# Kernel tuning notes

Hardware: AMD Instinct MI355X
Metric: run time of the kernel (lower is better)

## Reference

```python
import jax, jax.numpy as jnp
import numpy as np

NMS_THRESH = 0.5
SCORE_THRESH = 0.05
MAX_DET = 300


def _iou_one_vs_all(box, boxes):
    # box: [4] (x1,y1,x2,y2); boxes: [N,4]
    x1 = jnp.maximum(box[0], boxes[:, 0])
    y1 = jnp.maximum(box[1], boxes[:, 1])
    x2 = jnp.minimum(box[2], boxes[:, 2])
    y2 = jnp.minimum(box[3], boxes[:, 3])
    inter = jnp.maximum(x2 - x1, 0.0) * jnp.maximum(y2 - y1, 0.0)
    area_a = (box[2] - box[0]) * (box[3] - box[1])
    area_b = (boxes[:, 2] - boxes[:, 0]) * (boxes[:, 3] - boxes[:, 1])
    union = area_a + area_b - inter
    return inter / jnp.maximum(union, 1e-8)


def _nms_single_class(boxes, scores):
    # Greedy NMS with max_output_size=MAX_DET, matching tf.image.non_max_suppression
    # after score-threshold prefiltering. boxes:[N,4], scores:[N].
    s0 = jnp.where(scores > SCORE_THRESH, scores, -jnp.inf)

    def step(s, _):
        i = jnp.argmax(s)
        si = s[i]
        sel = jnp.isfinite(si)  # False once no candidates remain
        iou = _iou_one_vs_all(boxes[i], boxes)
        s = jnp.where(sel & (iou > NMS_THRESH), -jnp.inf, s)
        s = s.at[i].set(-jnp.inf)
        return s, (i, si, sel)

    _, (idx, sv, sel) = jax.lax.scan(step, s0, None, length=MAX_DET)
    # unselected slots carry -inf score
    return idx.astype(jnp.int32), jnp.where(sel, sv, -jnp.inf)


def _filter_one_image(boxes, classification, other):
    # boxes:[N,4], classification:[N,C], other:[N,D]
    C = classification.shape[1]
    # class-specific NMS (class_specific_filter=True, nms=True)
    idx, sv = jax.vmap(lambda c: _nms_single_class(boxes, classification[:, c]))(
        jnp.arange(C))  # each [C, MAX_DET]
    labels = jnp.broadcast_to(jnp.arange(C)[:, None], idx.shape)
    cand_scores = sv.reshape(-1)          # [C*MAX_DET]
    cand_idx = idx.reshape(-1)
    cand_lab = labels.reshape(-1)
    # global top-k over all per-class survivors
    top_s, top_i = jax.lax.top_k(cand_scores, MAX_DET)
    sel_idx = cand_idx[top_i]
    sel_lab = cand_lab[top_i]
    valid = jnp.isfinite(top_s)
    # pad invalid slots with -1 (matches tf.pad(..., constant_values=-1))
    out_boxes = jnp.where(valid[:, None], boxes[sel_idx], -1.0)
    out_scores = jnp.where(valid, top_s, -1.0)
    out_labels = jnp.where(valid, sel_lab, -1).astype(jnp.int32)
    out_other = jnp.where(valid[:, None], other[sel_idx], -1.0)
    return out_boxes, out_scores, out_labels, out_other


def setup_inputs() -> dict:
    key = jax.random.key(0)
    k1, k2, k3, k4 = jax.random.split(key, 4)
    B, N, C, D = 16, 50000, 8, 2
    xy = jax.random.uniform(k1, (B, N, 2), jnp.float32, 0.0, 512.0)
    wh = jax.random.uniform(k2, (B, N, 2), jnp.float32, 4.0, 100.0)
    boxes = jnp.concatenate([xy, xy + wh], axis=-1)  # valid (x1,y1,x2,y2)
    classification = jax.random.uniform(k3, (B, N, C), jnp.float32)
    other = jax.random.normal(k4, (B, N, D), jnp.float32)
    return {"boxes": boxes, "classification": classification, "other": other}


def reference(boxes, classification, other):
    # tf.map_fn over batch -> vmap over batch
    return jax.vmap(_filter_one_image)(boxes, classification, other)
```

## Files before the change

kernel.cpp:

```cpp
#include <hip/hip_runtime.h>
#include <math.h>
#include <stdint.h>

#define NB 16
#define NN 50000
#define NC 8
#define ND 2
#define MAX_DET 300
#define NMS_T 0.5f
#define SCORE_T 0.05f
#define CAP 1024
#define CUTBIN 252
#define LBUF 128
#define CHUNK 128
#define NT 512
#define NPI (NN * NC)
#define CBLK 32
#define F4PB (NPI / 4 / CBLK)

typedef unsigned long long u64;

__device__ __forceinline__ float neg_inf() { return -__builtin_inff(); }

__device__ __forceinline__ bool iou_gt(float ax1, float ay1, float ax2, float ay2,
                                       float area_a,
                                       float bx1, float by1, float bx2, float by2) {
    float x1 = fmaxf(ax1, bx1), y1 = fmaxf(ay1, by1);
    float x2 = fminf(ax2, bx2), y2 = fminf(ay2, by2);
    float inter = __fmul_rn(fmaxf(__fsub_rn(x2, x1), 0.0f),
                            fmaxf(__fsub_rn(y2, y1), 0.0f));
    float area_b = __fmul_rn(__fsub_rn(bx2, bx1), __fsub_rn(by2, by1));
    float uni = __fsub_rn(__fadd_rn(area_a, area_b), inter);
    return inter > __fmul_rn(0.5f, fmaxf(uni, 1e-8f));
}

__device__ __forceinline__ u64 score_key(float s, int n) {
    unsigned u = __float_as_uint(s);
    u ^= (u & 0x80000000u) ? 0xFFFFFFFFu : 0x80000000u;
    return ((u64)u << 32) | (unsigned)(~(unsigned)n);
}

__device__ __forceinline__ u64 shfl_xor_u64(u64 v, int m) {
    unsigned lo = (unsigned)v, hi = (unsigned)(v >> 32);
    lo = __shfl_xor(lo, m, 64);
    hi = __shfl_xor(hi, m, 64);
    return ((u64)hi << 32) | lo;
}

__global__ __launch_bounds__(1024) void compact_kernel(
    const float* __restrict__ cls, int* __restrict__ cnt_g,
    u64* __restrict__ cand)
{
    const int b = blockIdx.x >> 5, t32 = blockIdx.x & 31;
    const int tid = threadIdx.x;
    __shared__ u64 buf[8][LBUF];
    __shared__ int lcnt[8], gbase[8];
    if (tid < 8) lcnt[tid] = 0;
    __syncthreads();

    const float4* c4 = (const float4*)(cls + (size_t)b * NPI);
    const int f0 = t32 * F4PB, fend = f0 + F4PB;

    for (int f = f0 + tid; f < fend; f += 1024) {
        float4 v = c4[f];
        int cb = (f & 1) * 4;
        int n = f >> 1;
        float vv[4] = {v.x, v.y, v.z, v.w};
        #pragma unroll
        for (int k = 0; k < 4; ++k) {
            float s = vv[k];
            if (s > SCORE_T) {
                int bn = (int)(s * 256.0f); if (bn > 255) bn = 255;
                if (bn >= CUTBIN) {
                    int c = cb + k;
                    int pos = atomicAdd(&lcnt[c], 1);
                    u64 key = score_key(s, n);
                    if (pos < LBUF) buf[c][pos] = key;
                    else {
                        int gp = atomicAdd(&cnt_g[b * 8 + c], 1);
                        if (gp < CAP) cand[(size_t)(b * 8 + c) * CAP + gp] = key;
                    }
                }
            }
        }
    }
    __syncthreads();
    if (tid < 8) {
        int m = lcnt[tid]; if (m > LBUF) m = LBUF;
        gbase[tid] = atomicAdd(&cnt_g[b * 8 + tid], m);
    }
    __syncthreads();
    for (int c = 0; c < 8; ++c) {
        int m = lcnt[c]; if (m > LBUF) m = LBUF;
        int gb = gbase[c];
        for (int i = tid; i < m; i += 1024) {
            int gp = gb + i;
            if (gp < CAP) cand[(size_t)(b * 8 + c) * CAP + gp] = buf[c][i];
        }
    }
}

__global__ __launch_bounds__(NT) void nms_fused(
    const float* __restrict__ boxes, const float* __restrict__ cls,
    const u64* __restrict__ cand, const int* __restrict__ cnt_g,
    int* __restrict__ sel_idx, float* __restrict__ sel_score)
{
    const int bc = blockIdx.x;
    const int b = bc >> 3, c = bc & 7;
    const int tid = threadIdx.x;
    const int lane = tid & 63, widx = tid >> 6;
    const float4* bx4 = (const float4*)(boxes + (size_t)b * NN * 4);
    const float* sr = cls + (size_t)b * NN * NC + c;
    const u64* g = cand + (size_t)bc * CAP;
    int* si = sel_idx + bc * MAX_DET;
    float* ss = sel_score + bc * MAX_DET;

    __shared__ u64 keys[CAP];
    __shared__ float4 cbox2[2][CHUNK];
    __shared__ float  carea2[2][CHUNK];
    __shared__ int    cidx2[2][CHUNK];
    __shared__ float  cscore2[2][CHUNK];
    __shared__ unsigned M32[4][CHUNK];
    __shared__ unsigned presup4[4][CHUNK];
    __shared__ u64 accmask_s[2];
    __shared__ float4 abox[MAX_DET];
    __shared__ float aarea[MAX_DET];
    __shared__ unsigned bm[(NN + 31) / 32];
    __shared__ float rv[NT];
    __shared__ int   ri[NT];
    __shared__ float sboxsh[5];

    const int cnt = cnt_g[bc];
    const bool full_fb = (cnt > CAP);
    const int inSet = cnt < CAP ? cnt : CAP;

    int n_acc = 0;
    if (!full_fb) {
        const int p0 = widx * 128 + lane, p1 = p0 + 64;
        u64 v0 = (p0 < cnt) ? g[p0] : 0ull;
        u64 v1 = (p1 < cnt) ? g[p1] : 0ull;

        #pragma unroll
        for (int k = 2; k <= 128; k <<= 1) {
            #pragma unroll
            for (int j = k >> 1; j > 0; j >>= 1) {
                if (j == 64) {
                    bool dir = ((p0 & k) == 0);
                    if ((v0 < v1) == dir) { u64 t = v0; v0 = v1; v1 = t; }
                } else {
                    bool lower = ((lane & j) == 0);
                    bool dir0 = ((p0 & k) == 0);
                    bool dir1 = ((p1 & k) == 0);
                    u64 o0 = shfl_xor_u64(v0, j);
                    u64 mx0 = v0 > o0 ? v0 : o0, mn0 = v0 > o0 ? o0 : v0;
                    v0 = (lower == dir0) ? mx0 : mn0;
                    u64 o1 = shfl_xor_u64(v1, j);
                    u64 mx1 = v1 > o1 ? v1 : o1, mn1 = v1 > o1 ? o1 : v1;
                    v1 = (lower == dir1) ? mx1 : mn1;
                }
            }
        }
        for (int k = 256; k <= CAP; k <<= 1) {
            keys[p0] = v0; keys[p1] = v1;
            __syncthreads();
            for (int j = k >> 1; j >= 128; j >>= 1) {
                int p = tid;
                int i = 2 * p - (p & (j - 1));
                int ix = i + j;
                bool dir = ((i & k) == 0);
                u64 a = keys[i], b2 = keys[ix];
                if ((a < b2) == dir) { keys[i] = b2; keys[ix] = a; }
                __syncthreads();
            }
            v0 = keys[p0]; v1 = keys[p1];
            {
                bool dir = ((p0 & k) == 0);
                if ((v0 < v1) == dir) { u64 t = v0; v0 = v1; v1 = t; }
            }
            #pragma unroll
            for (int j = 32; j > 0; j >>= 1) {
                bool lower = ((lane & j) == 0);
                bool dir = ((p0 & k) == 0);
                u64 o0 = shfl_xor_u64(v0, j);
                u64 mx0 = v0 > o0 ? v0 : o0, mn0 = v0 > o0 ? o0 : v0;
                v0 = (lower == dir) ? mx0 : mn0;
                u64 o1 = shfl_xor_u64(v1, j);
                u64 mx1 = v1 > o1 ? v1 : o1, mn1 = v1 > o1 ? o1 : v1;
                v1 = (lower == dir) ? mx1 : mn1;
            }
            __syncthreads();
        }
        keys[p0] = v0; keys[p1] = v1;
        __syncthreads();

        if (tid < CHUNK && tid < inSet) {
            u64 key = keys[tid];
            int idx = (int)(~(unsigned)key);
            unsigned u = (unsigned)(key >> 32);
            unsigned uo = (u & 0x80000000u) ? (u ^ 0x80000000u) : (~u);
            float4 bb = bx4[idx];
            cbox2[0][tid] = bb;
            carea2[0][tid] = __fmul_rn(__fsub_rn(bb.z, bb.x), __fsub_rn(bb.w, bb.y));
            cidx2[0][tid] = idx; cscore2[0][tid] = __uint_as_float(uo);
        }
        __syncthreads();

        int base = 0, cur = 0;
        while (n_acc < MAX_DET && base < inSet) {
            int m = inSet - base; if (m > CHUNK) m = CHUNK;

            {
                int i = tid & (CHUNK - 1);
                int q = tid >> 7;
                if (i < m) {
                    float4 B = cbox2[cur][i];
                    unsigned p = 0;
                    int t = q;
                    for (; t + 12 < n_acc; t += 16) {
                        float4 A0 = abox[t];      float r0 = aarea[t];
                        float4 A1 = abox[t + 4];  float r1 = aarea[t + 4];
                        float4 A2 = abox[t + 8];  float r2 = aarea[t + 8];
                        float4 A3 = abox[t + 12]; float r3 = aarea[t + 12];
                        bool s0 = iou_gt(A0.x,A0.y,A0.z,A0.w,r0,B.x,B.y,B.z,B.w);
                        bool s1 = iou_gt(A1.x,A1.y,A1.z,A1.w,r1,B.x,B.y,B.z,B.w);
                        bool s2 = iou_gt(A2.x,A2.y,A2.z,A2.w,r2,B.x,B.y,B.z,B.w);
                        bool s3 = iou_gt(A3.x,A3.y,A3.z,A3.w,r3,B.x,B.y,B.z,B.w);
                        if (s0 || s1 || s2 || s3) { p = 1; break; }
                    }
                    if (!p) {
                        for (; t < n_acc; t += 4) {
                            float4 A = abox[t];
                            if (iou_gt(A.x,A.y,A.z,A.w,aarea[t],
                                       B.x,B.y,B.z,B.w)) { p = 1; break; }
                        }
                    }
                    presup4[q][i] = p;
                    unsigned bits = 0;
                    int j0 = q * 32;
                    int jend = i - j0; if (jend > 32) jend = 32;
                    for (int jj = 0; jj < jend; ++jj) {
                        int j = j0 + jj;
                        float4 A = cbox2[cur][j];
                        if (iou_gt(A.x,A.y,A.z,A.w,carea2[cur][j],
                                   B.x,B.y,B.z,B.w))
                            bits |= 1u << jj;
                    }
                    M32[q][i] = bits;
                }
            }
            __syncthreads();

            int nbase = base + m;
            if (tid < 64) {
                u64 a0 = 0, a1 = 0;
                int ngroups = (m + 63) >> 6;
                for (int gg = 0; gg < ngroups; ++gg) {
                    int i = gg * 64 + tid;
                    unsigned pe = 1; u64 mg = 0;
                    if (i < m) {
                        pe = presup4[0][i] | presup4[1][i] | presup4[2][i] | presup4[3][i];
                        mg = (u64)M32[2 * gg][i] | ((u64)M32[2 * gg + 1][i] << 32);
                        if (gg > 0) {
                            u64 w0 = (u64)M32[0][i] | ((u64)M32[1][i] << 32);
                            if (w0 & a0) pe = 1;
                        }
                    }
                    u64 rem = ~__ballot(pe != 0);
                    u64 accw = 0;
                    while (rem) {
                        int l = __builtin_ctzll(rem);
                        accw |= 1ull << l;
                        rem &= ~(1ull << l);
                        u64 supm = __ballot(((mg >> l) & 1ull) != 0);
                        rem &= ~supm;
                    }
                    if (gg == 0) a0 = accw; else a1 = accw;
                }
                if (tid == 0) { accmask_s[0] = a0; accmask_s[1] = a1; }
            } else if (nbase < inSet) {
                int w = tid - 64;
                if (w < CHUNK && nbase + w < inSet) {
                    u64 key = keys[nbase + w];
                    int idx = (int)(~(unsigned)key);
                    unsigned u = (unsigned)(key >> 32);
                    unsigned uo = (u & 0x80000000u) ? (u ^ 0x80000000u) : (~u);
                    float4 bb = bx4[idx];
                    cbox2[cur ^ 1][w] = bb;
                    carea2[cur ^ 1][w] = __fmul_rn(__fsub_rn(bb.z, bb.x), __fsub_rn(bb.w, bb.y));
                    cidx2[cur ^ 1][w] = idx; cscore2[cur ^ 1][w] = __uint_as_float(uo);
                }
            }
            __syncthreads();

            u64 a0 = accmask_s[0], a1 = accmask_s[1];
            int add = __popcll(a0) + __popcll(a1);
            if (tid < m) {
                int gg = tid >> 6, o = tid & 63;
                u64 aw = (gg == 0) ? a0 : a1;
                if ((aw >> o) & 1ull) {
                    int rank = (gg > 0) ? __popcll(a0) : 0;
                    rank += __popcll(aw & ((1ull << o) - 1ull));
                    int pos = n_acc + rank;
                    if (pos < MAX_DET) {
                        abox[pos] = cbox2[cur][tid]; aarea[pos] = carea2[cur][tid];
                        si[pos] = cidx2[cur][tid]; ss[pos] = cscore2[cur][tid];
                    }
                }
            }
            n_acc += add; if (n_acc > MAX_DET) n_acc = MAX_DET;
            base = nbase; cur ^= 1;
            __syncthreads();
        }
    }

    const bool part_fb = (!full_fb) && (n_acc < MAX_DET);

    if (full_fb || part_fb) {
        const int BMW = (NN + 31) / 32;
        for (int i = tid; i < BMW; i += NT) bm[i] = 0u;
        __syncthreads();
        if (full_fb) {
            n_acc = 0;
        } else {
            for (int n = tid; n < NN; n += NT) {
                float4 bbn = bx4[n];
                int s = 0;
                for (int t = 0; t < n_acc; ++t) {
                    float4 A = abox[t];
                    if (iou_gt(A.x, A.y, A.z, A.w, aarea[t],
                               bbn.x, bbn.y, bbn.z, bbn.w)) s = 1;
                }
                if (s) atomicOr(&bm[n >> 5], 1u << (n & 31));
            }
        }
        __syncthreads();

        for (int k = n_acc; k < MAX_DET; ++k) {
            float bv = neg_inf(); int bi = 0x7fffffff;
            for (int n = tid; n < NN; n += NT) {
                if (!((bm[n >> 5] >> (n & 31)) & 1u)) {
                    float v = sr[(size_t)n * NC];
                    if (v > SCORE_T && v > bv) { bv = v; bi = n; }
                }
            }
            rv[tid] = bv; ri[tid] = bi;
            __syncthreads();
            for (int s = NT / 2; s > 0; s >>= 1) {
                if (tid < s) {
                    float ov = rv[tid + s]; int oi = ri[tid + s];
                    if (ov > rv[tid] || (ov == rv[tid] && oi < ri[tid])) { rv[tid] = ov; ri[tid] = oi; }
                }
                __syncthreads();
            }
            float mval = rv[0]; int midx = ri[0];
            if (mval == neg_inf()) {
                for (int kk = k + tid; kk < MAX_DET; kk += NT) { si[kk] = 0; ss[kk] = neg_inf(); }
                break;
            }
            if (tid == 0) {
                si[k] = midx; ss[k] = mval;
                float4 sb = bx4[midx];
                sboxsh[0] = sb.x; sboxsh[1] = sb.y; sboxsh[2] = sb.z; sboxsh[3] = sb.w;
                sboxsh[4] = __fmul_rn(__fsub_rn(sb.z, sb.x), __fsub_rn(sb.w, sb.y));
            }
            __syncthreads();
            float ax1 = sboxsh[0], ay1 = sboxsh[1], ax2 = sboxsh[2], ay2 = sboxsh[3];
            float area_a = sboxsh[4];
            for (int n = tid; n < NN; n += NT) {
                float4 bbn = bx4[n];
                if (iou_gt(ax1, ay1, ax2, ay2, area_a,
                           bbn.x, bbn.y, bbn.z, bbn.w))
                    atomicOr(&bm[n >> 5], 1u << (n & 31));
            }
            __syncthreads();
        }
    } else {
        for (int kk = n_acc + tid; kk < MAX_DET; kk += NT) { si[kk] = 0; ss[kk] = neg_inf(); }
    }
}

__global__ __launch_bounds__(1024) void topk_kernel(
    const float* __restrict__ boxes, const float* __restrict__ other,
    const int* __restrict__ sel_idx, const float* __restrict__ sel_score,
    float* __restrict__ out)
{
    const int b = blockIdx.x;
    const int tid = threadIdx.x;
    __shared__ u64 keys[4096];

    for (int i = tid; i < 4096; i += 1024) {
        int c = i >> 9, o = i & 511;
        u64 key = 0ull;
        if (o < MAX_DET) {
            int m = c * MAX_DET + o;
            float v = sel_score[b * NC * MAX_DET + m];
            unsigned u = __float_as_uint(v);
            u ^= (u & 0x80000000u) ? 0xFFFFFFFFu : 0x80000000u;
            key = ((u64)u << 32) | (unsigned)(~(unsigned)m);
        }
        keys[i] = key;
    }

    for (int seg = 1024; seg <= 4096; seg <<= 1) {
        int half = seg >> 1;
        __syncthreads();
        {
            int p = tid;
            int s = p / (half >> 1), t = p % (half >> 1);
            int i0 = s * seg + half + t;
            int i1 = s * seg + seg - 1 - t;
            u64 a = keys[i0]; keys[i0] = keys[i1]; keys[i1] = a;
        }
        __syncthreads();
        for (int j = half; j > 0; j >>= 1) {
            for (int p = tid; p < 2048; p += 1024) {
                int i = 2 * p - (p & (j - 1));
                int ix = i + j;
                u64 a = keys[i], bq = keys[ix];
                if (a < bq) { keys[i] = bq; keys[ix] = a; }
            }
            if (j >= 128) __syncthreads(); else __threadfence_block();
        }
    }
    __syncthreads();

    const float4* bx4 = (const float4*)(boxes + (size_t)b * NN * 4);
    const float*  ot  = other + (size_t)b * NN * ND;
    float* ob = out;
    float* os = out + NB * MAX_DET * 4;
    float* ol = os + NB * MAX_DET;
    float* oo = ol + NB * MAX_DET;

    for (int k = tid; k < MAX_DET; k += 1024) {
        u64 key = keys[k];
        unsigned u = (unsigned)(key >> 32);
        unsigned uo = (u & 0x80000000u) ? (u ^ 0x80000000u) : (u ^ 0xFFFFFFFFu);
        float score = __uint_as_float(uo);
        bool valid = isfinite(score);
        float b0=-1.f,b1=-1.f,b2=-1.f,b3=-1.f,scv=-1.f,lab=-1.f,o0=-1.f,o1=-1.f;
        if (valid) {
            int m = (int)(~(unsigned)key);
            int c = m / MAX_DET, slot = m - c * MAX_DET;
            int n = sel_idx[(b * NC + c) * MAX_DET + slot];
            float4 bb = bx4[n];
            b0 = bb.x; b1 = bb.y; b2 = bb.z; b3 = bb.w;
            scv = score; lab = (float)c;
            o0 = ot[n * ND + 0]; o1 = ot[n * ND + 1];
        }
        int base = b * MAX_DET + k;
        ob[base * 4 + 0] = b0; ob[base * 4 + 1] = b1;
        ob[base * 4 + 2] = b2; ob[base * 4 + 3] = b3;
        os[base] = scv; ol[base] = lab;
        oo[base * 2 + 0] = o0; oo[base * 2 + 1] = o1;
    }
}

extern "C" void kernel_launch(void* const* d_in, const int* in_sizes, int n_in,
                              void* d_out, int out_size, void* d_ws, size_t ws_size,
                              hipStream_t stream) {
    const float* boxes = (const float*)d_in[0];
    const float* cls   = (const float*)d_in[1];
    const float* other = (const float*)d_in[2];
    float* out = (float*)d_out;

    int* cnt_g = (int*)d_ws;
    u64* cand  = (u64*)(cnt_g + NB * NC * 2);
    int* sel_idx = (int*)(cand + (size_t)NB * NC * CAP);
    float* sel_score = (float*)(sel_idx + NB * NC * MAX_DET);

    hipMemsetAsync(cnt_g, 0, NB * NC * sizeof(int), stream);
    compact_kernel<<<NB * CBLK, 1024, 0, stream>>>(cls, cnt_g, cand);
    nms_fused<<<NB * NC, NT, 0, stream>>>(boxes, cls, cand, cnt_g,
                                          sel_idx, sel_score);
    topk_kernel<<<NB, 1024, 0, stream>>>(boxes, other, sel_idx, sel_score, out);
}
```

Measured before the change: 72.74 us.

## Resolve first 512 NMS candidates in one block-wide suppression-matrix pass

```diff
diff --git a/kernel.cpp b/kernel.cpp
--- a/kernel.cpp
+++ b/kernel.cpp
@@ -12,6 +12,7 @@
 #define CAP 1024
 #define CUTBIN 252
 #define LBUF 128
+#define BIGM 512
 #define CHUNK 128
 #define NT 512
 #define NPI (NN * NC)
@@ -116,19 +117,28 @@
     float* ss = sel_score + bc * MAX_DET;
 
     __shared__ u64 keys[CAP];
-    __shared__ float4 cbox2[2][CHUNK];
-    __shared__ float  carea2[2][CHUNK];
-    __shared__ int    cidx2[2][CHUNK];
-    __shared__ float  cscore2[2][CHUNK];
-    __shared__ unsigned M32[4][CHUNK];
-    __shared__ unsigned presup4[4][CHUNK];
+    __shared__ __align__(16) char regA[32768];
+    __shared__ __align__(16) char regB[14336];
+    __shared__ u64 accs_s[8];
     __shared__ u64 accmask_s[2];
     __shared__ float4 abox[MAX_DET];
     __shared__ float aarea[MAX_DET];
-    __shared__ unsigned bm[(NN + 31) / 32];
-    __shared__ float rv[NT];
-    __shared__ int   ri[NT];
     __shared__ float sboxsh[5];
+
+    u64 (*Mword)[BIGM] = (u64(*)[BIGM])regA;
+    unsigned* bm = (unsigned*)regA;
+    float* rv = (float*)(regA + 6256);
+    int*   ri = (int*)(regA + 8304);
+    float4* cbig   = (float4*)regB;
+    float* careabig = (float*)(regB + 8192);
+    int*   cidxbig  = (int*)(regB + 10240);
+    float* csbig    = (float*)(regB + 12288);
+    float4 (*cbox2)[CHUNK] = (float4(*)[CHUNK])regB;
+    float*  carea2 = (float*)(regB + 4096);
+    int*    cidx2  = (int*)(regB + 5120);
+    float*  cscore2= (float*)(regB + 6144);
+    unsigned (*M32)[CHUNK] = (unsigned(*)[CHUNK])(regB + 7168);
+    unsigned (*presup4)[CHUNK] = (unsigned(*)[CHUNK])(regB + 9216);
 
     const int cnt = cnt_g[bc];
     const bool full_fb = (cnt > CAP);
@@ -139,7 +149,6 @@
         const int p0 = widx * 128 + lane, p1 = p0 + 64;
         u64 v0 = (p0 < cnt) ? g[p0] : 0ull;
         u64 v1 = (p1 < cnt) ? g[p1] : 0ull;
-
         #pragma unroll
         for (int k = 2; k <= 128; k <<= 1) {
             #pragma unroll
@@ -193,123 +202,192 @@
         keys[p0] = v0; keys[p1] = v1;
         __syncthreads();
 
-        if (tid < CHUNK && tid < inSet) {
+        const int stage = inSet < BIGM ? inSet : BIGM;
+        if (tid < stage) {
             u64 key = keys[tid];
             int idx = (int)(~(unsigned)key);
             unsigned u = (unsigned)(key >> 32);
             unsigned uo = (u & 0x80000000u) ? (u ^ 0x80000000u) : (~u);
             float4 bb = bx4[idx];
-            cbox2[0][tid] = bb;
-            carea2[0][tid] = __fmul_rn(__fsub_rn(bb.z, bb.x), __fsub_rn(bb.w, bb.y));
-            cidx2[0][tid] = idx; cscore2[0][tid] = __uint_as_float(uo);
-        }
-        __syncthreads();
-
-        int base = 0, cur = 0;
-        while (n_acc < MAX_DET && base < inSet) {
-            int m = inSet - base; if (m > CHUNK) m = CHUNK;
-
-            {
-                int i = tid & (CHUNK - 1);
-                int q = tid >> 7;
-                if (i < m) {
-                    float4 B = cbox2[cur][i];
-                    unsigned p = 0;
-                    int t = q;
-                    for (; t + 12 < n_acc; t += 16) {
-                        float4 A0 = abox[t];      float r0 = aarea[t];
-                        float4 A1 = abox[t + 4];  float r1 = aarea[t + 4];
-                        float4 A2 = abox[t + 8];  float r2 = aarea[t + 8];
-                        float4 A3 = abox[t + 12]; float r3 = aarea[t + 12];
-                        bool s0 = iou_gt(A0.x,A0.y,A0.z,A0.w,r0,B.x,B.y,B.z,B.w);
-                        bool s1 = iou_gt(A1.x,A1.y,A1.z,A1.w,r1,B.x,B.y,B.z,B.w);
-                        bool s2 = iou_gt(A2.x,A2.y,A2.z,A2.w,r2,B.x,B.y,B.z,B.w);
-                        bool s3 = iou_gt(A3.x,A3.y,A3.z,A3.w,r3,B.x,B.y,B.z,B.w);
-                        if (s0 || s1 || s2 || s3) { p = 1; break; }
+            cbig[tid] = bb;
+            careabig[tid] = __fmul_rn(__fsub_rn(bb.z, bb.x), __fsub_rn(bb.w, bb.y));
+            cidxbig[tid] = idx; csbig[tid] = __uint_as_float(uo);
+        }
+        __syncthreads();
+
+        {
+            const int r = tid;
+            const int jmax = (widx + 1) << 6;
+            float4 B = cbig[r < stage ? r : 0];
+            float  Ba = careabig[r < stage ? r : 0];
+            (void)Ba;
+            u64 bits = 0;
+            for (int j = 0; j < jmax; ++j) {
+                if (j < r && r < stage) {
+                    float4 A = cbig[j];
+                    if (iou_gt(A.x, A.y, A.z, A.w, careabig[j],
+                               B.x, B.y, B.z, B.w))
+                        bits |= 1ull << (j & 63);
+                }
+                if ((j & 63) == 63) { Mword[j >> 6][r] = bits; bits = 0; }
+            }
+        }
+        __syncthreads();
+
+        if (tid < 64) {
+            u64 acc[8];
+            #pragma unroll
+            for (int gg = 0; gg < 8; ++gg) acc[gg] = 0ull;
+            const int stage = inSet < BIGM ? inSet : BIGM;
+            for (int gg = 0; gg < 8; ++gg) {
+                int i = gg * 64 + lane;
+                unsigned pe = (i < stage) ? 0u : 1u;
+                u64 mg = 0;
+                if (i < stage) {
+                    mg = Mword[gg][i];
+                    for (int h = 0; h < gg; ++h)
+                        if (Mword[h][i] & acc[h]) pe = 1;
+                }
+                u64 rem = ~__ballot(pe != 0);
+                u64 accw = 0;
+                while (rem) {
+                    int l = __builtin_ctzll(rem);
+                    accw |= 1ull << l;
+                    rem &= ~(1ull << l);
+                    u64 supm = __ballot(((mg >> l) & 1ull) != 0);
+                    rem &= ~supm;
+                }
+                acc[gg] = accw;
+            }
+            if (lane == 0) {
+                #pragma unroll
+                for (int gg = 0; gg < 8; ++gg) accs_s[gg] = acc[gg];
+            }
+        }
+        __syncthreads();
+
+        {
+            int total_acc = 0;
+            #pragma unroll
+            for (int gg = 0; gg < 8; ++gg) total_acc += __popcll(accs_s[gg]);
+            int gg = widx, o = 0;
+            gg = tid >> 6; o = tid & 63;
+            u64 aw = accs_s[gg];
+            if ((aw >> o) & 1ull) {
+                int rank = 0;
+                for (int h = 0; h < gg; ++h) rank += __popcll(accs_s[h]);
+                rank += __popcll(aw & ((1ull << o) - 1ull));
+                if (rank < MAX_DET) {
+                    abox[rank] = cbig[tid]; aarea[rank] = careabig[tid];
+                    si[rank] = cidxbig[tid]; ss[rank] = csbig[tid];
+                }
+            }
+            n_acc = total_acc < MAX_DET ? total_acc : MAX_DET;
+        }
+        __syncthreads();
+
+        int base = BIGM, cur = 0;
+        if (n_acc < MAX_DET && base < inSet) {
+            if (tid < CHUNK && base + tid < inSet) {
+                u64 key = keys[base + tid];
+                int idx = (int)(~(unsigned)key);
+                unsigned u = (unsigned)(key >> 32);
+                unsigned uo = (u & 0x80000000u) ? (u ^ 0x80000000u) : (~u);
+                float4 bb = bx4[idx];
+                cbox2[0][tid] = bb;
+                carea2[0 * CHUNK + tid] = __fmul_rn(__fsub_rn(bb.z, bb.x), __fsub_rn(bb.w, bb.y));
+                cidx2[0 * CHUNK + tid] = idx; cscore2[0 * CHUNK + tid] = __uint_as_float(uo);
+            }
+            __syncthreads();
+            while (n_acc < MAX_DET && base < inSet) {
+                int m = inSet - base; if (m > CHUNK) m = CHUNK;
+                {
+                    int i = tid & (CHUNK - 1);
+                    int q = tid >> 7;
+                    if (i < m) {
+                        float4 B = cbox2[cur][i];
+                        unsigned p = 0;
+                        for (int t = q; t < n_acc; t += 4) {
+                            float4 A = abox[t];
+                            if (iou_gt(A.x, A.y, A.z, A.w, aarea[t],
+                                       B.x, B.y, B.z, B.w)) { p = 1; break; }
+                        }
+                        presup4[q][i] = p;
+                        unsigned bits = 0;
+                        int j0 = q * 32;
+                        int jend = i - j0; if (jend > 32) jend = 32;
+                        for (int jj = 0; jj < jend; ++jj) {
+                            int j = j0 + jj;
+                            float4 A = cbox2[cur][j];
+                            if (iou_gt(A.x, A.y, A.z, A.w, carea2[cur * CHUNK + j],
+                                       B.x, B.y, B.z, B.w))
+                                bits |= 1u << jj;
+                        }
+                        M32[q][i] = bits;
                     }
-                    if (!p) {
-                        for (; t < n_acc; t += 4) {
-                            float4 A = abox[t];
-                            if (iou_gt(A.x,A.y,A.z,A.w,aarea[t],
-                                       B.x,B.y,B.z,B.w)) { p = 1; break; }
+                }
+                __syncthreads();
+                int nbase = base + m;
+                if (tid < 64) {
+                    u64 a0 = 0, a1 = 0;
+                    int ngroups = (m + 63) >> 6;
+                    for (int gg = 0; gg < ngroups; ++gg) {
+                        int i = gg * 64 + lane;
+                        unsigned pe = 1; u64 mg = 0;
+                        if (i < m) {
+                            pe = presup4[0][i] | presup4[1][i] | presup4[2][i] | presup4[3][i];
+                            mg = (u64)M32[2 * gg][i] | ((u64)M32[2 * gg + 1][i] << 32);
+                            if (gg > 0) {
+                                u64 w0 = (u64)M32[0][i] | ((u64)M32[1][i] << 32);
+                                if (w0 & a0) pe = 1;
+                            }
+                        }
+                        u64 rem = ~__ballot(pe != 0);
+                        u64 accw = 0;
+                        while (rem) {
+                            int l = __builtin_ctzll(rem);
+                            accw |= 1ull << l;
+                            rem &= ~(1ull << l);
+                            u64 supm = __ballot(((mg >> l) & 1ull) != 0);
+                            rem &= ~supm;
+                        }
+                        if (gg == 0) a0 = accw; else a1 = accw;
+                    }
+                    if (lane == 0) { accmask_s[0] = a0; accmask_s[1] = a1; }
+                } else if (nbase < inSet) {
+                    int w = tid - 64;
+                    if (w < CHUNK && nbase + w < inSet) {
+                        u64 key = keys[nbase + w];
+                        int idx = (int)(~(unsigned)key);
+                        unsigned u = (unsigned)(key >> 32);
+                        unsigned uo = (u & 0x80000000u) ? (u ^ 0x80000000u) : (~u);
+                        float4 bb = bx4[idx];
+                        cbox2[cur ^ 1][w] = bb;
+                        carea2[(cur ^ 1) * CHUNK + w] = __fmul_rn(__fsub_rn(bb.z, bb.x), __fsub_rn(bb.w, bb.y));
+                        cidx2[(cur ^ 1) * CHUNK + w] = idx;
+                        cscore2[(cur ^ 1) * CHUNK + w] = __uint_as_float(uo);
+                    }
+                }
+                __syncthreads();
+                u64 a0 = accmask_s[0], a1 = accmask_s[1];
+                int add = __popcll(a0) + __popcll(a1);
+                if (tid < m) {
+                    int gg = tid >> 6, o = tid & 63;
+                    u64 aw = (gg == 0) ? a0 : a1;
+                    if ((aw >> o) & 1ull) {
+                        int rank = (gg > 0) ? __popcll(a0) : 0;
+                        rank += __popcll(aw & ((1ull << o) - 1ull));
+                        int pos = n_acc + rank;
+                        if (pos < MAX_DET) {
+                            abox[pos] = cbox2[cur][tid]; aarea[pos] = carea2[cur * CHUNK + tid];
+                            si[pos] = cidx2[cur * CHUNK + tid]; ss[pos] = cscore2[cur * CHUNK + tid];
                         }
                     }
-                    presup4[q][i] = p;
-                    unsigned bits = 0;
-                    int j0 = q * 32;
-                    int jend = i - j0; if (jend > 32) jend = 32;
-                    for (int jj = 0; jj < jend; ++jj) {
-                        int j = j0 + jj;
-                        float4 A = cbox2[cur][j];
-                        if (iou_gt(A.x,A.y,A.z,A.w,carea2[cur][j],
-                                   B.x,B.y,B.z,B.w))
-                            bits |= 1u << jj;
-                    }
-                    M32[q][i] = bits;
-                }
-            }
-            __syncthreads();
-
-            int nbase = base + m;
-            if (tid < 64) {
-                u64 a0 = 0, a1 = 0;
-                int ngroups = (m + 63) >> 6;
-                for (int gg = 0; gg < ngroups; ++gg) {
-                    int i = gg * 64 + tid;
-                    unsigned pe = 1; u64 mg = 0;
-                    if (i < m) {
-                        pe = presup4[0][i] | presup4[1][i] | presup4[2][i] | presup4[3][i];
-                        mg = (u64)M32[2 * gg][i] | ((u64)M32[2 * gg + 1][i] << 32);
-                        if (gg > 0) {
-                            u64 w0 = (u64)M32[0][i] | ((u64)M32[1][i] << 32);
-                            if (w0 & a0) pe = 1;
-                        }
-                    }
-                    u64 rem = ~__ballot(pe != 0);
-                    u64 accw = 0;
-                    while (rem) {
-                        int l = __builtin_ctzll(rem);
-                        accw |= 1ull << l;
-                        rem &= ~(1ull << l);
-                        u64 supm = __ballot(((mg >> l) & 1ull) != 0);
-                        rem &= ~supm;
-                    }
-                    if (gg == 0) a0 = accw; else a1 = accw;
-                }
-                if (tid == 0) { accmask_s[0] = a0; accmask_s[1] = a1; }
-            } else if (nbase < inSet) {
-                int w = tid - 64;
-                if (w < CHUNK && nbase + w < inSet) {
-                    u64 key = keys[nbase + w];
-                    int idx = (int)(~(unsigned)key);
-                    unsigned u = (unsigned)(key >> 32);
-                    unsigned uo = (u & 0x80000000u) ? (u ^ 0x80000000u) : (~u);
-                    float4 bb = bx4[idx];
-                    cbox2[cur ^ 1][w] = bb;
-                    carea2[cur ^ 1][w] = __fmul_rn(__fsub_rn(bb.z, bb.x), __fsub_rn(bb.w, bb.y));
-                    cidx2[cur ^ 1][w] = idx; cscore2[cur ^ 1][w] = __uint_as_float(uo);
-                }
-            }
-            __syncthreads();
-
-            u64 a0 = accmask_s[0], a1 = accmask_s[1];
-            int add = __popcll(a0) + __popcll(a1);
-            if (tid < m) {
-                int gg = tid >> 6, o = tid & 63;
-                u64 aw = (gg == 0) ? a0 : a1;
-                if ((aw >> o) & 1ull) {
-                    int rank = (gg > 0) ? __popcll(a0) : 0;
-                    rank += __popcll(aw & ((1ull << o) - 1ull));
-                    int pos = n_acc + rank;
-                    if (pos < MAX_DET) {
-                        abox[pos] = cbox2[cur][tid]; aarea[pos] = carea2[cur][tid];
-                        si[pos] = cidx2[cur][tid]; ss[pos] = cscore2[cur][tid];
-                    }
-                }
-            }
-            n_acc += add; if (n_acc > MAX_DET) n_acc = MAX_DET;
-            base = nbase; cur ^= 1;
-            __syncthreads();
+                }
+                n_acc += add; if (n_acc > MAX_DET) n_acc = MAX_DET;
+                base = nbase; cur ^= 1;
+                __syncthreads();
+            }
         }
     }
 
```

New measurement: 128.4 us. 76.6% more time.

## Replace global-atomic candidate compaction with per-tile slots and in-NMS prefix scan

Applied to the files above, without the earlier changes.

```diff
diff --git a/kernel.cpp b/kernel.cpp
--- a/kernel.cpp
+++ b/kernel.cpp
@@ -12,11 +12,11 @@
 #define CAP 1024
 #define CUTBIN 252
 #define LBUF 128
+#define NTILE32 32
 #define CHUNK 128
 #define NT 512
 #define NPI (NN * NC)
-#define CBLK 32
-#define F4PB (NPI / 4 / CBLK)
+#define F4PB (NPI / 4 / NTILE32)
 
 typedef unsigned long long u64;
 
@@ -48,13 +48,13 @@
 }
 
 __global__ __launch_bounds__(1024) void compact_kernel(
-    const float* __restrict__ cls, int* __restrict__ cnt_g,
+    const float* __restrict__ cls, int* __restrict__ tcnt_g,
     u64* __restrict__ cand)
 {
     const int b = blockIdx.x >> 5, t32 = blockIdx.x & 31;
     const int tid = threadIdx.x;
     __shared__ u64 buf[8][LBUF];
-    __shared__ int lcnt[8], gbase[8];
+    __shared__ int lcnt[8];
     if (tid < 8) lcnt[tid] = 0;
     __syncthreads();
 
@@ -74,35 +74,24 @@
                 if (bn >= CUTBIN) {
                     int c = cb + k;
                     int pos = atomicAdd(&lcnt[c], 1);
-                    u64 key = score_key(s, n);
-                    if (pos < LBUF) buf[c][pos] = key;
-                    else {
-                        int gp = atomicAdd(&cnt_g[b * 8 + c], 1);
-                        if (gp < CAP) cand[(size_t)(b * 8 + c) * CAP + gp] = key;
-                    }
+                    if (pos < LBUF) buf[c][pos] = score_key(s, n);
                 }
             }
         }
     }
     __syncthreads();
-    if (tid < 8) {
-        int m = lcnt[tid]; if (m > LBUF) m = LBUF;
-        gbase[tid] = atomicAdd(&cnt_g[b * 8 + tid], m);
-    }
-    __syncthreads();
-    for (int c = 0; c < 8; ++c) {
-        int m = lcnt[c]; if (m > LBUF) m = LBUF;
-        int gb = gbase[c];
-        for (int i = tid; i < m; i += 1024) {
-            int gp = gb + i;
-            if (gp < CAP) cand[(size_t)(b * 8 + c) * CAP + gp] = buf[c][i];
-        }
+    {
+        int c = tid >> 7, i = tid & (LBUF - 1);
+        int m = lcnt[c];
+        if (i < (m < LBUF ? m : LBUF))
+            cand[(size_t)(((b * 8 + c) * NTILE32) + t32) * LBUF + i] = buf[c][i];
+        if (i == 0) tcnt_g[(b * 8 + c) * NTILE32 + t32] = m;
     }
 }
 
 __global__ __launch_bounds__(NT) void nms_fused(
     const float* __restrict__ boxes, const float* __restrict__ cls,
-    const u64* __restrict__ cand, const int* __restrict__ cnt_g,
+    const u64* __restrict__ cand, const int* __restrict__ tcnt_g,
     int* __restrict__ sel_idx, float* __restrict__ sel_score)
 {
     const int bc = blockIdx.x;
@@ -111,11 +100,12 @@
     const int lane = tid & 63, widx = tid >> 6;
     const float4* bx4 = (const float4*)(boxes + (size_t)b * NN * 4);
     const float* sr = cls + (size_t)b * NN * NC + c;
-    const u64* g = cand + (size_t)bc * CAP;
     int* si = sel_idx + bc * MAX_DET;
     float* ss = sel_score + bc * MAX_DET;
 
     __shared__ u64 keys[CAP];
+    __shared__ int tcnt_s[NTILE32], toff_s[NTILE32];
+    __shared__ int sh_total, sh_ovf;
     __shared__ float4 cbox2[2][CHUNK];
     __shared__ float  carea2[2][CHUNK];
     __shared__ int    cidx2[2][CHUNK];
@@ -130,16 +120,37 @@
     __shared__ int   ri[NT];
     __shared__ float sboxsh[5];
 
-    const int cnt = cnt_g[bc];
-    const bool full_fb = (cnt > CAP);
+    if (tid < 64) {
+        int v = (lane < NTILE32) ? tcnt_g[bc * NTILE32 + lane] : 0;
+        int incl = v;
+        #pragma unroll
+        for (int d = 1; d < 32; d <<= 1) {
+            int o = __shfl_up(incl, d, 64);
+            if (lane >= d) incl += o;
+        }
+        if (lane < NTILE32) { tcnt_s[lane] = v; toff_s[lane] = incl - v; }
+        u64 ov = __ballot(lane < NTILE32 && v > LBUF);
+        if (lane == 31) { sh_total = incl; sh_ovf = (ov != 0); }
+    }
+    __syncthreads();
+    const int cnt = sh_total;
+    const bool full_fb = sh_ovf || (cnt > CAP);
     const int inSet = cnt < CAP ? cnt : CAP;
 
     int n_acc = 0;
     if (!full_fb) {
+        for (int i = tid; i < CAP; i += NT) keys[i] = 0ull;
+        __syncthreads();
+        for (int s = tid; s < NTILE32 * LBUF; s += NT) {
+            int t = s >> 7, i = s & (LBUF - 1);
+            if (i < tcnt_s[t])
+                keys[toff_s[t] + i] = cand[(size_t)(bc * NTILE32 + t) * LBUF + i];
+        }
+        __syncthreads();
+
         const int p0 = widx * 128 + lane, p1 = p0 + 64;
-        u64 v0 = (p0 < cnt) ? g[p0] : 0ull;
-        u64 v1 = (p1 < cnt) ? g[p1] : 0ull;
-
+        u64 v0 = keys[p0];
+        u64 v1 = keys[p1];
         #pragma unroll
         for (int k = 2; k <= 128; k <<= 1) {
             #pragma unroll
@@ -160,6 +171,7 @@
                 }
             }
         }
+        __syncthreads();
         for (int k = 256; k <= CAP; k <<= 1) {
             keys[p0] = v0; keys[p1] = v1;
             __syncthreads();
@@ -238,12 +250,23 @@
                     unsigned bits = 0;
                     int j0 = q * 32;
                     int jend = i - j0; if (jend > 32) jend = 32;
-                    for (int jj = 0; jj < jend; ++jj) {
+                    int jj = 0;
+                    for (; jj + 3 < jend; jj += 4) {
+                        int j = j0 + jj;
+                        float4 A0 = cbox2[cur][j];     float r0 = carea2[cur][j];
+                        float4 A1 = cbox2[cur][j + 1]; float r1 = carea2[cur][j + 1];
+                        float4 A2 = cbox2[cur][j + 2]; float r2 = carea2[cur][j + 2];
+                        float4 A3 = cbox2[cur][j + 3]; float r3 = carea2[cur][j + 3];
+                        if (iou_gt(A0.x,A0.y,A0.z,A0.w,r0,B.x,B.y,B.z,B.w)) bits |= 1u << jj;
+                        if (iou_gt(A1.x,A1.y,A1.z,A1.w,r1,B.x,B.y,B.z,B.w)) bits |= 1u << (jj+1);
+                        if (iou_gt(A2.x,A2.y,A2.z,A2.w,r2,B.x,B.y,B.z,B.w)) bits |= 1u << (jj+2);
+                        if (iou_gt(A3.x,A3.y,A3.z,A3.w,r3,B.x,B.y,B.z,B.w)) bits |= 1u << (jj+3);
+                    }
+                    for (; jj < jend; ++jj) {
                         int j = j0 + jj;
                         float4 A = cbox2[cur][j];
                         if (iou_gt(A.x,A.y,A.z,A.w,carea2[cur][j],
-                                   B.x,B.y,B.z,B.w))
-                            bits |= 1u << jj;
+                                   B.x,B.y,B.z,B.w)) bits |= 1u << jj;
                     }
                     M32[q][i] = bits;
                 }
@@ -255,7 +278,7 @@
                 u64 a0 = 0, a1 = 0;
                 int ngroups = (m + 63) >> 6;
                 for (int gg = 0; gg < ngroups; ++gg) {
-                    int i = gg * 64 + tid;
+                    int i = gg * 64 + lane;
                     unsigned pe = 1; u64 mg = 0;
                     if (i < m) {
                         pe = presup4[0][i] | presup4[1][i] | presup4[2][i] | presup4[3][i];
@@ -276,7 +299,7 @@
                     }
                     if (gg == 0) a0 = accw; else a1 = accw;
                 }
-                if (tid == 0) { accmask_s[0] = a0; accmask_s[1] = a1; }
+                if (lane == 0) { accmask_s[0] = a0; accmask_s[1] = a1; }
             } else if (nbase < inSet) {
                 int w = tid - 64;
                 if (w < CHUNK && nbase + w < inSet) {
@@ -463,14 +486,13 @@
     const float* other = (const float*)d_in[2];
     float* out = (float*)d_out;
 
-    int* cnt_g = (int*)d_ws;
-    u64* cand  = (u64*)(cnt_g + NB * NC * 2);
-    int* sel_idx = (int*)(cand + (size_t)NB * NC * CAP);
+    int* tcnt_g = (int*)d_ws;
+    u64* cand  = (u64*)(tcnt_g + NB * NC * NTILE32);
+    int* sel_idx = (int*)(cand + (size_t)NB * NC * NTILE32 * LBUF);
     float* sel_score = (float*)(sel_idx + NB * NC * MAX_DET);
 
-    hipMemsetAsync(cnt_g, 0, NB * NC * sizeof(int), stream);
-    compact_kernel<<<NB * CBLK, 1024, 0, stream>>>(cls, cnt_g, cand);
-    nms_fused<<<NB * NC, NT, 0, stream>>>(boxes, cls, cand, cnt_g,
+    compact_kernel<<<NB * NTILE32, 1024, 0, stream>>>(cls, tcnt_g, cand);
+    nms_fused<<<NB * NC, NT, 0, stream>>>(boxes, cls, cand, tcnt_g,
                                           sel_idx, sel_score);
     topk_kernel<<<NB, 1024, 0, stream>>>(boxes, other, sel_idx, sel_score, out);
 }
```

After: 67.16 us. 1.08x faster.
